# Kernel tuning notes

Hardware: AMD Instinct MI355X
Metric: run time of the kernel (lower is better)

## Reference

```python
import jax, jax.numpy as jnp
import numpy as np

N_NODES = 50000
N_EDGES = 800000
IN_FEATS = 128
H_FEATS = 64
NUM_CLASSES = 2
K = 3
LAMBDA_MAX = 2.0  # standard upper bound for normalized-Laplacian max eigenvalue


def setup_inputs() -> dict:
    key = jax.random.key(0)
    ks = jax.random.split(key, 16)
    s = 0.05
    return {
        "in_feat": jax.random.normal(ks[0], (N_NODES, IN_FEATS), jnp.float32),
        "src": jax.random.randint(ks[1], (N_EDGES,), 0, N_NODES, jnp.int32),
        "dst": jax.random.randint(ks[2], (N_EDGES,), 0, N_NODES, jnp.int32),
        "W1": jax.random.normal(ks[3], (H_FEATS, IN_FEATS), jnp.float32) * s,
        "b1": jnp.zeros((H_FEATS,), jnp.float32),
        "W2": jax.random.normal(ks[4], (H_FEATS, H_FEATS), jnp.float32) * s,
        "b2": jnp.zeros((H_FEATS,), jnp.float32),
        "Wc1": jax.random.normal(ks[5], (H_FEATS, K * H_FEATS), jnp.float32) * s,
        "bc1": jnp.zeros((H_FEATS,), jnp.float32),
        "Wc2": jax.random.normal(ks[6], (H_FEATS, K * H_FEATS), jnp.float32) * s,
        "bc2": jnp.zeros((H_FEATS,), jnp.float32),
        "W3": jax.random.normal(ks[7], (H_FEATS, H_FEATS), jnp.float32) * s,
        "b3": jnp.zeros((H_FEATS,), jnp.float32),
        "W4": jax.random.normal(ks[8], (NUM_CLASSES, H_FEATS), jnp.float32) * s,
        "b4": jnp.zeros((NUM_CLASSES,), jnp.float32),
    }


def _cheb_conv(h, src, dst, d_invsqrt, W, b, k):
    """DGL ChebConv: Chebyshev recursion on scaled normalized Laplacian,
    concat k terms along feature dim, then Linear + relu (default activation)."""
    n = h.shape[0]
    re_norm = 2.0 / LAMBDA_MAX

    def a_norm(x):  # D^{-1/2} A D^{-1/2} x via edge-list SpMM
        msg = (x * d_invsqrt)[src]                              # [E, F]
        agg = jax.ops.segment_sum(msg, dst, num_segments=n)     # [N, F]
        return agg * d_invsqrt

    X0 = h
    Xs = [X0]
    X1 = -re_norm * a_norm(X0) + X0 * (re_norm - 1.0)
    Xs.append(X1)
    for _ in range(2, k):
        Xi = -2.0 * re_norm * a_norm(X1) + X1 * (2.0 * (re_norm - 1.0)) - X0
        Xs.append(Xi)
        X0, X1 = X1, Xi
    Xt = jnp.concatenate(Xs, axis=1)                            # [N, k*F]
    return jax.nn.relu(Xt @ W.T + b)


def reference(in_feat, src, dst, W1, b1, W2, b2, Wc1, bc1, Wc2, bc2, W3, b3, W4, b4):
    n = in_feat.shape[0]
    # in-degrees from dst, clamp(min=1), D^{-1/2}
    deg = jax.ops.segment_sum(jnp.ones_like(dst, jnp.float32), dst, num_segments=n)
    d_invsqrt = jnp.power(jnp.maximum(deg, 1.0), -0.5)[:, None]  # [N, 1]

    h = jax.nn.relu(in_feat @ W1.T + b1)
    h = jax.nn.relu(h @ W2.T + b2)
    h = _cheb_conv(h, src, dst, d_invsqrt, Wc1, bc1, K)
    h = _cheb_conv(h, src, dst, d_invsqrt, Wc2, bc2, K)
    h = jax.nn.relu(h @ W3.T + b3)
    h = h @ W4.T + b4
    return h
```

## Files before the change

kernel.cpp:

```cpp
#include <hip/hip_runtime.h>
#include <hip/hip_fp16.h>
#include <math.h>

#define NN 50000
#define NE 800000
#define INF 128
#define H 64
#define ELLCAP 64
#define NPART 8
#define PSIZE ((NN + NPART - 1) / NPART)
#define EPT 25
#define CHUNK (256 * EPT)
#define NCHUNK ((NE + CHUNK - 1) / CHUNK)
#define NB_FILL (NCHUNK * NPART)
#define NB_G ((NN + 63) / 64)
#define WOFF_W1 0
#define WOFF_W2 8192
#define WOFF_WC1 12288
#define WOFF_WC2 24576
#define WOFF_W3 36864
#define WTOT 40960
#define NB_CVTW (WTOT / 2048)
#define NB_DINV 25

typedef _Float16 half8_t __attribute__((ext_vector_type(8)));
typedef float float4_t __attribute__((ext_vector_type(4)));

__device__ __forceinline__ half8_t load_cvt8(const float* p) {
  float4 a = *(const float4*)(p);
  float4 b = *(const float4*)(p + 4);
  half8_t h;
  h[0] = (_Float16)a.x; h[1] = (_Float16)a.y; h[2] = (_Float16)a.z; h[3] = (_Float16)a.w;
  h[4] = (_Float16)b.x; h[5] = (_Float16)b.y; h[6] = (_Float16)b.z; h[7] = (_Float16)b.w;
  return h;
}

__global__ __launch_bounds__(256) void k_prep(const int* __restrict__ src, const int* __restrict__ dst,
                                              int* __restrict__ cnt, unsigned short* __restrict__ ell,
                                              const float* __restrict__ W1, const float* __restrict__ W2,
                                              const float* __restrict__ Wc1, const float* __restrict__ Wc2,
                                              const float* __restrict__ W3, _Float16* __restrict__ w16) {
  int b = blockIdx.x;
  if (b < NB_FILL) {
    int p = b & (NPART - 1);
    int chunk = b >> 3;
    int lo = p * PSIZE, hi = lo + PSIZE;
    int base = chunk * CHUNK + threadIdx.x;
#pragma unroll
    for (int i = 0; i < EPT; ++i) {
      int e = base + i * 256;
      if (e < NE) {
        int d = __builtin_nontemporal_load(&dst[e]);
        if (d >= lo && d < hi) {
          int s = __builtin_nontemporal_load(&src[e]);
          int c = atomicAdd(&cnt[d], 1);
          if (c < ELLCAP) ell[((size_t)d << 6) + c] = (unsigned short)s;
        }
      }
    }
  } else {
    int i0 = (b - NB_FILL) * 2048 + threadIdx.x * 8;
#pragma unroll
    for (int k = 0; k < 8; ++k) {
      int id = i0 + k;
      if (id < WTOT) {
        float v;
        if (id < WOFF_W2) v = W1[id];
        else if (id < WOFF_WC1) v = W2[id - WOFF_W2];
        else if (id < WOFF_WC2) v = Wc1[id - WOFF_WC1];
        else if (id < WOFF_W3) v = Wc2[id - WOFF_WC2];
        else v = W3[id - WOFF_W3];
        w16[id] = (_Float16)v;
      }
    }
  }
}

__global__ __launch_bounds__(256) void k_mlp(const float* __restrict__ in_feat,
                                             const _Float16* __restrict__ w16,
                                             const float* __restrict__ b1,
                                             const float* __restrict__ b2,
                                             const int* __restrict__ cnt,
                                             float* __restrict__ dinv32,
                                             _Float16* __restrict__ X0c, int N) {
  __shared__ _Float16 Hs[64][72];
  if (blockIdx.x < NB_DINV) {
    int i0 = blockIdx.x * 2048 + threadIdx.x * 8;
#pragma unroll
    for (int k = 0; k < 8; ++k) {
      int i = i0 + k;
      if (i < N) {
        int c = cnt[i];
        dinv32[i] = 1.0f / sqrtf((float)(c < 1 ? 1 : c));
      }
    }
    return;
  }
  const int tid = threadIdx.x;
  const int wave = tid >> 6;
  const int lane = tid & 63;
  const int m = lane & 15;
  const int quad = lane >> 4;
  const int rbase = (blockIdx.x - NB_DINV) * 64 + wave * 16;
  int arow = rbase + m;
  arow = arow < N ? arow : N - 1;
  const float* Ap = in_feat + (size_t)arow * INF + quad * 8;
  const _Float16* B1 = w16 + WOFF_W1 + (size_t)m * INF + quad * 8;
  float4_t acc[4] = {{0.f,0.f,0.f,0.f},{0.f,0.f,0.f,0.f},{0.f,0.f,0.f,0.f},{0.f,0.f,0.f,0.f}};
#pragma unroll
  for (int k0 = 0; k0 < INF; k0 += 32) {
    half8_t a = load_cvt8(Ap + k0);
    half8_t b0 = *(const half8_t*)(B1 + k0);
    half8_t b1f = *(const half8_t*)(B1 + 16 * INF + k0);
    half8_t b2f = *(const half8_t*)(B1 + 32 * INF + k0);
    half8_t b3f = *(const half8_t*)(B1 + 48 * INF + k0);
    acc[0] = __builtin_amdgcn_mfma_f32_16x16x32_f16(a, b0, acc[0], 0, 0, 0);
    acc[1] = __builtin_amdgcn_mfma_f32_16x16x32_f16(a, b1f, acc[1], 0, 0, 0);
    acc[2] = __builtin_amdgcn_mfma_f32_16x16x32_f16(a, b2f, acc[2], 0, 0, 0);
    acc[3] = __builtin_amdgcn_mfma_f32_16x16x32_f16(a, b3f, acc[3], 0, 0, 0);
  }
#pragma unroll
  for (int i = 0; i < 4; ++i)
#pragma unroll
    for (int t = 0; t < 4; ++t)
      Hs[wave * 16 + quad * 4 + i][t * 16 + m] = (_Float16)fmaxf(acc[t][i] + b1[t * 16 + m], 0.f);
  __syncthreads();
  const _Float16* Ap2 = &Hs[wave * 16 + m][quad * 8];
  const _Float16* B2 = w16 + WOFF_W2 + (size_t)m * H + quad * 8;
  float4_t acc2[4] = {{0.f,0.f,0.f,0.f},{0.f,0.f,0.f,0.f},{0.f,0.f,0.f,0.f},{0.f,0.f,0.f,0.f}};
#pragma unroll
  for (int k0 = 0; k0 < H; k0 += 32) {
    half8_t a = *(const half8_t*)(Ap2 + k0);
    half8_t b0 = *(const half8_t*)(B2 + k0);
    half8_t b1f = *(const half8_t*)(B2 + 16 * H + k0);
    half8_t b2f = *(const half8_t*)(B2 + 32 * H + k0);
    half8_t b3f = *(const half8_t*)(B2 + 48 * H + k0);
    acc2[0] = __builtin_amdgcn_mfma_f32_16x16x32_f16(a, b0, acc2[0], 0, 0, 0);
    acc2[1] = __builtin_amdgcn_mfma_f32_16x16x32_f16(a, b1f, acc2[1], 0, 0, 0);
    acc2[2] = __builtin_amdgcn_mfma_f32_16x16x32_f16(a, b2f, acc2[2], 0, 0, 0);
    acc2[3] = __builtin_amdgcn_mfma_f32_16x16x32_f16(a, b3f, acc2[3], 0, 0, 0);
  }
#pragma unroll
  for (int i = 0; i < 4; ++i) {
    int rr = rbase + quad * 4 + i;
    if (rr < N) {
#pragma unroll
      for (int t = 0; t < 4; ++t)
        X0c[((size_t)rr << 6) + t * 16 + m] = (_Float16)fmaxf(acc2[t][i] + b2[t * 16 + m], 0.f);
    }
  }
}

__global__ __launch_bounds__(256) void k_spmm(const _Float16* __restrict__ table,
                                              const _Float16* __restrict__ auxc,
                                              _Float16* __restrict__ outc,
                                              const int* __restrict__ cnt,
                                              const float* __restrict__ dinv32,
                                              const unsigned short* __restrict__ ell,
                                              float alpha, int use_aux, int N) {
  int wv = (blockIdx.x * 256 + threadIdx.x) >> 6;
  int lane = threadIdx.x & 63;
  int node = wv * 4 + (lane >> 4);
  if (node >= N) return;
  int g = (lane >> 3) & 1;
  int c8 = (lane & 7) * 8;
  int deg0 = cnt[node];
  int deg = deg0 < ELLCAP ? deg0 : ELLCAP;
  const unsigned short* row = ell + ((size_t)node << 6);

  float acc[8] = {0.f, 0.f, 0.f, 0.f, 0.f, 0.f, 0.f, 0.f};
  int j = g;
  for (; j + 2 < deg; j += 4) {
    int s0 = row[j];
    int s1 = row[j + 2];
    float d0 = dinv32[s0];
    float d1 = dinv32[s1];
    half8_t v0 = *(const half8_t*)(table + ((size_t)s0 << 6) + c8);
    half8_t v1 = *(const half8_t*)(table + ((size_t)s1 << 6) + c8);
#pragma unroll
    for (int k = 0; k < 8; ++k) acc[k] = fmaf(d0, (float)v0[k], fmaf(d1, (float)v1[k], acc[k]));
  }
  if (j < deg) {
    int s0 = row[j];
    float d0 = dinv32[s0];
    half8_t v0 = *(const half8_t*)(table + ((size_t)s0 << 6) + c8);
#pragma unroll
    for (int k = 0; k < 8; ++k) acc[k] = fmaf(d0, (float)v0[k], acc[k]);
  }
#pragma unroll
  for (int k = 0; k < 8; ++k) acc[k] += __shfl_xor(acc[k], 8);
  if (g == 0) {
    float a = alpha * dinv32[node];
    float r[8];
#pragma unroll
    for (int k = 0; k < 8; ++k) r[k] = a * acc[k];
    if (use_aux) {
      half8_t x = *(const half8_t*)(auxc + ((size_t)node << 6) + c8);
#pragma unroll
      for (int k = 0; k < 8; ++k) r[k] -= (float)x[k];
    }
    half8_t ro;
#pragma unroll
    for (int k = 0; k < 8; ++k) ro[k] = (_Float16)r[k];
    *(half8_t*)(outc + ((size_t)node << 6) + c8) = ro;
  }
}

__global__ __launch_bounds__(256) void k_gemm192(const _Float16* __restrict__ A0,
                                                 const _Float16* __restrict__ A1,
                                                 const _Float16* __restrict__ A2,
                                                 const _Float16* __restrict__ B,
                                                 const float* __restrict__ bias,
                                                 _Float16* __restrict__ outc, int N) {
  const int tid = threadIdx.x;
  const int wave = tid >> 6;
  const int lane = tid & 63;
  const int m = lane & 15;
  const int quad = lane >> 4;
  const int rbase = blockIdx.x * 64 + wave * 16;
  int arow = rbase + m;
  arow = arow < N ? arow : N - 1;
  const size_t ro = ((size_t)arow << 6) + quad * 8;
  const _Float16* Bp = B + (size_t)m * 192 + quad * 8;
  float4_t acc[4] = {{0.f,0.f,0.f,0.f},{0.f,0.f,0.f,0.f},{0.f,0.f,0.f,0.f},{0.f,0.f,0.f,0.f}};
#pragma unroll
  for (int k0 = 0; k0 < 192; k0 += 32) {
    half8_t a;
    if (k0 < 64) a = *(const half8_t*)(A0 + ro + k0);
    else if (k0 < 128) a = *(const half8_t*)(A1 + ro + (k0 - 64));
    else a = *(const half8_t*)(A2 + ro + (k0 - 128));
    half8_t b0 = *(const half8_t*)(Bp + k0);
    half8_t b1f = *(const half8_t*)(Bp + 16 * 192 + k0);
    half8_t b2f = *(const half8_t*)(Bp + 32 * 192 + k0);
    half8_t b3f = *(const half8_t*)(Bp + 48 * 192 + k0);
    acc[0] = __builtin_amdgcn_mfma_f32_16x16x32_f16(a, b0, acc[0], 0, 0, 0);
    acc[1] = __builtin_amdgcn_mfma_f32_16x16x32_f16(a, b1f, acc[1], 0, 0, 0);
    acc[2] = __builtin_amdgcn_mfma_f32_16x16x32_f16(a, b2f, acc[2], 0, 0, 0);
    acc[3] = __builtin_amdgcn_mfma_f32_16x16x32_f16(a, b3f, acc[3], 0, 0, 0);
  }
#pragma unroll
  for (int i = 0; i < 4; ++i) {
    int rr = rbase + quad * 4 + i;
    if (rr < N) {
#pragma unroll
      for (int t = 0; t < 4; ++t)
        outc[((size_t)rr << 6) + t * 16 + m] = (_Float16)fmaxf(acc[t][i] + bias[t * 16 + m], 0.f);
    }
  }
}

__global__ __launch_bounds__(256) void k_tail(const _Float16* __restrict__ A0,
                                              const _Float16* __restrict__ A1,
                                              const _Float16* __restrict__ A2,
                                              const _Float16* __restrict__ w16,
                                              const float* __restrict__ bc2,
                                              const float* __restrict__ b3,
                                              const float* __restrict__ W4,
                                              const float* __restrict__ b4,
                                              float* __restrict__ out, int N) {
  __shared__ _Float16 Hs2[64][72];
  __shared__ float Hs3[64][65];
  const int tid = threadIdx.x;
  const int wave = tid >> 6;
  const int lane = tid & 63;
  const int m = lane & 15;
  const int quad = lane >> 4;
  const int rbase = blockIdx.x * 64 + wave * 16;
  int arow = rbase + m;
  arow = arow < N ? arow : N - 1;
  {
    const size_t ro = ((size_t)arow << 6) + quad * 8;
    const _Float16* Bp = w16 + WOFF_WC2 + (size_t)m * 192 + quad * 8;
    float4_t acc[4] = {{0.f,0.f,0.f,0.f},{0.f,0.f,0.f,0.f},{0.f,0.f,0.f,0.f},{0.f,0.f,0.f,0.f}};
#pragma unroll
    for (int k0 = 0; k0 < 192; k0 += 32) {
      half8_t a;
      if (k0 < 64) a = *(const half8_t*)(A0 + ro + k0);
      else if (k0 < 128) a = *(const half8_t*)(A1 + ro + (k0 - 64));
      else a = *(const half8_t*)(A2 + ro + (k0 - 128));
      half8_t b0 = *(const half8_t*)(Bp + k0);
      half8_t b1f = *(const half8_t*)(Bp + 16 * 192 + k0);
      half8_t b2f = *(const half8_t*)(Bp + 32 * 192 + k0);
      half8_t b3f = *(const half8_t*)(Bp + 48 * 192 + k0);
      acc[0] = __builtin_amdgcn_mfma_f32_16x16x32_f16(a, b0, acc[0], 0, 0, 0);
      acc[1] = __builtin_amdgcn_mfma_f32_16x16x32_f16(a, b1f, acc[1], 0, 0, 0);
      acc[2] = __builtin_amdgcn_mfma_f32_16x16x32_f16(a, b2f, acc[2], 0, 0, 0);
      acc[3] = __builtin_amdgcn_mfma_f32_16x16x32_f16(a, b3f, acc[3], 0, 0, 0);
    }
#pragma unroll
    for (int i = 0; i < 4; ++i)
#pragma unroll
      for (int t = 0; t < 4; ++t)
        Hs2[wave * 16 + quad * 4 + i][t * 16 + m] =
            (_Float16)fmaxf(acc[t][i] + bc2[t * 16 + m], 0.f);
  }
  __syncthreads();
  {
    const _Float16* Ap = &Hs2[wave * 16 + m][quad * 8];
    const _Float16* Bp = w16 + WOFF_W3 + (size_t)m * H + quad * 8;
    float4_t acc[4] = {{0.f,0.f,0.f,0.f},{0.f,0.f,0.f,0.f},{0.f,0.f,0.f,0.f},{0.f,0.f,0.f,0.f}};
#pragma unroll
    for (int k0 = 0; k0 < H; k0 += 32) {
      half8_t a = *(const half8_t*)(Ap + k0);
      half8_t b0 = *(const half8_t*)(Bp + k0);
      half8_t b1f = *(const half8_t*)(Bp + 16 * H + k0);
      half8_t b2f = *(const half8_t*)(Bp + 32 * H + k0);
      half8_t b3f = *(const half8_t*)(Bp + 48 * H + k0);
      acc[0] = __builtin_amdgcn_mfma_f32_16x16x32_f16(a, b0, acc[0], 0, 0, 0);
      acc[1] = __builtin_amdgcn_mfma_f32_16x16x32_f16(a, b1f, acc[1], 0, 0, 0);
      acc[2] = __builtin_amdgcn_mfma_f32_16x16x32_f16(a, b2f, acc[2], 0, 0, 0);
      acc[3] = __builtin_amdgcn_mfma_f32_16x16x32_f16(a, b3f, acc[3], 0, 0, 0);
    }
#pragma unroll
    for (int i = 0; i < 4; ++i)
#pragma unroll
      for (int t = 0; t < 4; ++t)
        Hs3[wave * 16 + quad * 4 + i][t * 16 + m] = fmaxf(acc[t][i] + b3[t * 16 + m], 0.f);
  }
  __syncthreads();
  if (tid < 128) {
    int r = tid >> 1;
    int c = tid & 1;
    int row = blockIdx.x * 64 + r;
    if (row < N) {
      const float* w4 = W4 + c * 64;
      float s = 0.f;
#pragma unroll
      for (int k = 0; k < 64; ++k) s = fmaf(Hs3[r][k], w4[k], s);
      out[(size_t)row * 2 + c] = s + b4[c];
    }
  }
}

extern "C" void kernel_launch(void* const* d_in, const int* in_sizes, int n_in,
                              void* d_out, int out_size, void* d_ws, size_t ws_size,
                              hipStream_t stream) {
  const float* in_feat = (const float*)d_in[0];
  const int* src = (const int*)d_in[1];
  const int* dst = (const int*)d_in[2];
  const float* W1 = (const float*)d_in[3];
  const float* b1 = (const float*)d_in[4];
  const float* W2 = (const float*)d_in[5];
  const float* b2 = (const float*)d_in[6];
  const float* Wc1 = (const float*)d_in[7];
  const float* bc1 = (const float*)d_in[8];
  const float* Wc2 = (const float*)d_in[9];
  const float* bc2 = (const float*)d_in[10];
  const float* W3 = (const float*)d_in[11];
  const float* b3 = (const float*)d_in[12];
  const float* W4 = (const float*)d_in[13];
  const float* b4 = (const float*)d_in[14];
  float* out = (float*)d_out;

  char* ws = (char*)d_ws;
  size_t o = 0;
  auto carve = [&](size_t bytes) -> void* {
    o = (o + 255) & ~(size_t)255;
    void* p = ws + o;
    o += bytes;
    return p;
  };
  int* cnt = (int*)carve((size_t)NN * 4);
  unsigned short* ell = (unsigned short*)carve((size_t)NN * ELLCAP * 2);
  float* dinv32 = (float*)carve((size_t)NN * 4);
  _Float16* w16 = (_Float16*)carve((size_t)WTOT * 2);
  _Float16* X0c = (_Float16*)carve((size_t)NN * H * 2);
  _Float16* X1c = (_Float16*)carve((size_t)NN * H * 2);
  _Float16* X2c = (_Float16*)carve((size_t)NN * H * 2);
  _Float16* Y0c = (_Float16*)carve((size_t)NN * H * 2);
  _Float16* Y1c = (_Float16*)carve((size_t)NN * H * 2);
  _Float16* Y2c = (_Float16*)carve((size_t)NN * H * 2);
  (void)ws_size; (void)in_sizes; (void)n_in; (void)out_size;

  const int NB_W4 = (NN + 15) / 16;
  const int NB_PREP = NB_FILL + NB_CVTW;

  hipMemsetAsync(cnt, 0, (size_t)NN * 4, stream);
  k_prep<<<NB_PREP, 256, 0, stream>>>(src, dst, cnt, ell, W1, W2, Wc1, Wc2, W3, w16);
  k_mlp<<<NB_DINV + NB_G, 256, 0, stream>>>(in_feat, w16, b1, b2, cnt, dinv32, X0c, NN);
  k_spmm<<<NB_W4, 256, 0, stream>>>(X0c, (const _Float16*)nullptr, X1c, cnt, dinv32, ell, -1.f, 0, NN);
  k_spmm<<<NB_W4, 256, 0, stream>>>(X1c, X0c, X2c, cnt, dinv32, ell, -2.f, 1, NN);
  k_gemm192<<<NB_G, 256, 0, stream>>>(X0c, X1c, X2c, w16 + WOFF_WC1, bc1, Y0c, NN);
  k_spmm<<<NB_W4, 256, 0, stream>>>(Y0c, (const _Float16*)nullptr, Y1c, cnt, dinv32, ell, -1.f, 0, NN);
  k_spmm<<<NB_W4, 256, 0, stream>>>(Y1c, Y0c, Y2c, cnt, dinv32, ell, -2.f, 1, NN);
  k_tail<<<NB_G, 256, 0, stream>>>(Y0c, Y1c, Y2c, w16, bc2, b3, W4, b4, out, NN);
}
```

Measured before the change: 269.2 us.

## Build ELL adjacency via two-pass bucket binning with shared-memory atomics

```diff
diff --git a/kernel.cpp b/kernel.cpp
--- a/kernel.cpp
+++ b/kernel.cpp
@@ -7,12 +7,6 @@
 #define INF 128
 #define H 64
 #define ELLCAP 64
-#define NPART 8
-#define PSIZE ((NN + NPART - 1) / NPART)
-#define EPT 25
-#define CHUNK (256 * EPT)
-#define NCHUNK ((NE + CHUNK - 1) / CHUNK)
-#define NB_FILL (NCHUNK * NPART)
 #define NB_G ((NN + 63) / 64)
 #define WOFF_W1 0
 #define WOFF_W2 8192
@@ -21,7 +15,13 @@
 #define WOFF_W3 36864
 #define WTOT 40960
 #define NB_CVTW (WTOT / 2048)
-#define NB_DINV 25
+
+#define PSHIFT 8
+#define NPART2 196
+#define CAP 8192
+#define NB_BINA 128
+#define EPB (NE / NB_BINA)
+#define EPT_A 25
 
 typedef _Float16 half8_t __attribute__((ext_vector_type(8)));
 typedef float float4_t __attribute__((ext_vector_type(4)));
@@ -35,31 +35,14 @@
   return h;
 }
 
-__global__ __launch_bounds__(256) void k_prep(const int* __restrict__ src, const int* __restrict__ dst,
-                                              int* __restrict__ cnt, unsigned short* __restrict__ ell,
+__global__ __launch_bounds__(256) void k_binA(const int* __restrict__ src, const int* __restrict__ dst,
+                                              int* __restrict__ gcount, int* __restrict__ bucket,
                                               const float* __restrict__ W1, const float* __restrict__ W2,
                                               const float* __restrict__ Wc1, const float* __restrict__ Wc2,
                                               const float* __restrict__ W3, _Float16* __restrict__ w16) {
   int b = blockIdx.x;
-  if (b < NB_FILL) {
-    int p = b & (NPART - 1);
-    int chunk = b >> 3;
-    int lo = p * PSIZE, hi = lo + PSIZE;
-    int base = chunk * CHUNK + threadIdx.x;
-#pragma unroll
-    for (int i = 0; i < EPT; ++i) {
-      int e = base + i * 256;
-      if (e < NE) {
-        int d = __builtin_nontemporal_load(&dst[e]);
-        if (d >= lo && d < hi) {
-          int s = __builtin_nontemporal_load(&src[e]);
-          int c = atomicAdd(&cnt[d], 1);
-          if (c < ELLCAP) ell[((size_t)d << 6) + c] = (unsigned short)s;
-        }
-      }
-    }
-  } else {
-    int i0 = (b - NB_FILL) * 2048 + threadIdx.x * 8;
+  if (b >= NB_BINA) {
+    int i0 = (b - NB_BINA) * 2048 + threadIdx.x * 8;
 #pragma unroll
     for (int k = 0; k < 8; ++k) {
       int id = i0 + k;
@@ -73,6 +56,78 @@
         w16[id] = (_Float16)v;
       }
     }
+    return;
+  }
+  __shared__ int s_cnt[NPART2];
+  __shared__ int s_base[NPART2];
+  const int tid = threadIdx.x;
+  if (tid < NPART2) s_cnt[tid] = 0;
+  __syncthreads();
+  const int e0 = b * EPB;
+  int rec[EPT_A];
+  int meta[EPT_A];
+#pragma unroll
+  for (int i = 0; i < EPT_A; ++i) {
+    int off = i * 256 + tid;
+    meta[i] = -1;
+    if (off < EPB) {
+      int e = e0 + off;
+      int d = __builtin_nontemporal_load(&dst[e]);
+      int s = __builtin_nontemporal_load(&src[e]);
+      int p = d >> PSHIFT;
+      rec[i] = s | ((d & 255) << 16);
+      int slot = atomicAdd(&s_cnt[p], 1);
+      meta[i] = (p << 13) | slot;
+    }
+  }
+  __syncthreads();
+  if (tid < NPART2) s_base[tid] = atomicAdd(&gcount[tid], s_cnt[tid]);
+  __syncthreads();
+#pragma unroll
+  for (int i = 0; i < EPT_A; ++i) {
+    if (meta[i] >= 0) {
+      int p = meta[i] >> 13;
+      int pos = s_base[p] + (meta[i] & 8191);
+      if (pos < CAP) bucket[(size_t)p * CAP + pos] = rec[i];
+    }
+  }
+}
+
+__global__ __launch_bounds__(256) void k_binB(const int* __restrict__ gcount, const int* __restrict__ bucket,
+                                              unsigned short* __restrict__ ell, int* __restrict__ cnt,
+                                              float* __restrict__ dinv32) {
+  __shared__ int s_cnt[256];
+  const int tid = threadIdx.x;
+  const int p = blockIdx.x;
+  s_cnt[tid] = 0;
+  __syncthreads();
+  int n = gcount[p];
+  n = n < CAP ? n : CAP;
+  const int* bp = bucket + (size_t)p * CAP;
+  int j = tid;
+  for (; j + 3 * 256 < n; j += 4 * 256) {
+    int r0 = bp[j], r1 = bp[j + 256], r2 = bp[j + 512], r3 = bp[j + 768];
+    int c0 = atomicAdd(&s_cnt[r0 >> 16], 1);
+    int c1 = atomicAdd(&s_cnt[r1 >> 16], 1);
+    int c2 = atomicAdd(&s_cnt[r2 >> 16], 1);
+    int c3 = atomicAdd(&s_cnt[r3 >> 16], 1);
+    if (c0 < ELLCAP) ell[((size_t)((p << PSHIFT) + (r0 >> 16)) << 6) + c0] = (unsigned short)(r0 & 0xFFFF);
+    if (c1 < ELLCAP) ell[((size_t)((p << PSHIFT) + (r1 >> 16)) << 6) + c1] = (unsigned short)(r1 & 0xFFFF);
+    if (c2 < ELLCAP) ell[((size_t)((p << PSHIFT) + (r2 >> 16)) << 6) + c2] = (unsigned short)(r2 & 0xFFFF);
+    if (c3 < ELLCAP) ell[((size_t)((p << PSHIFT) + (r3 >> 16)) << 6) + c3] = (unsigned short)(r3 & 0xFFFF);
+  }
+  for (; j < n; j += 256) {
+    int r = bp[j];
+    int dl = r >> 16;
+    int c = atomicAdd(&s_cnt[dl], 1);
+    if (c < ELLCAP) ell[((size_t)((p << PSHIFT) + dl) << 6) + c] = (unsigned short)(r & 0xFFFF);
+  }
+  __syncthreads();
+  int node = (p << PSHIFT) + tid;
+  if (node < NN) {
+    int c = s_cnt[tid];
+    cnt[node] = c;
+    dinv32[node] = 1.0f / sqrtf((float)(c < 1 ? 1 : c));
   }
 }
 
@@ -80,28 +135,14 @@
                                              const _Float16* __restrict__ w16,
                                              const float* __restrict__ b1,
                                              const float* __restrict__ b2,
-                                             const int* __restrict__ cnt,
-                                             float* __restrict__ dinv32,
                                              _Float16* __restrict__ X0c, int N) {
   __shared__ _Float16 Hs[64][72];
-  if (blockIdx.x < NB_DINV) {
-    int i0 = blockIdx.x * 2048 + threadIdx.x * 8;
-#pragma unroll
-    for (int k = 0; k < 8; ++k) {
-      int i = i0 + k;
-      if (i < N) {
-        int c = cnt[i];
-        dinv32[i] = 1.0f / sqrtf((float)(c < 1 ? 1 : c));
-      }
-    }
-    return;
-  }
   const int tid = threadIdx.x;
   const int wave = tid >> 6;
   const int lane = tid & 63;
   const int m = lane & 15;
   const int quad = lane >> 4;
-  const int rbase = (blockIdx.x - NB_DINV) * 64 + wave * 16;
+  const int rbase = blockIdx.x * 64 + wave * 16;
   int arow = rbase + m;
   arow = arow < N ? arow : N - 1;
   const float* Ap = in_feat + (size_t)arow * INF + quad * 8;
@@ -370,14 +411,16 @@
   _Float16* Y0c = (_Float16*)carve((size_t)NN * H * 2);
   _Float16* Y1c = (_Float16*)carve((size_t)NN * H * 2);
   _Float16* Y2c = (_Float16*)carve((size_t)NN * H * 2);
+  int* gcount = (int*)carve((size_t)NPART2 * 4);
+  int* bucket = (int*)Y0c;
   (void)ws_size; (void)in_sizes; (void)n_in; (void)out_size;
 
   const int NB_W4 = (NN + 15) / 16;
-  const int NB_PREP = NB_FILL + NB_CVTW;
-
-  hipMemsetAsync(cnt, 0, (size_t)NN * 4, stream);
-  k_prep<<<NB_PREP, 256, 0, stream>>>(src, dst, cnt, ell, W1, W2, Wc1, Wc2, W3, w16);
-  k_mlp<<<NB_DINV + NB_G, 256, 0, stream>>>(in_feat, w16, b1, b2, cnt, dinv32, X0c, NN);
+
+  hipMemsetAsync(gcount, 0, (size_t)NPART2 * 4, stream);
+  k_binA<<<NB_BINA + NB_CVTW, 256, 0, stream>>>(src, dst, gcount, bucket, W1, W2, Wc1, Wc2, W3, w16);
+  k_binB<<<NPART2, 256, 0, stream>>>(gcount, bucket, ell, cnt, dinv32);
+  k_mlp<<<NB_G, 256, 0, stream>>>(in_feat, w16, b1, b2, X0c, NN);
   k_spmm<<<NB_W4, 256, 0, stream>>>(X0c, (const _Float16*)nullptr, X1c, cnt, dinv32, ell, -1.f, 0, NN);
   k_spmm<<<NB_W4, 256, 0, stream>>>(X1c, X0c, X2c, cnt, dinv32, ell, -2.f, 1, NN);
   k_gemm192<<<NB_G, 256, 0, stream>>>(X0c, X1c, X2c, w16 + WOFF_WC1, bc1, Y0c, NN);
```

Result: faster. 242.8 us (-9.8%).
